# Kernel tuning notes

Hardware: AMD Instinct MI355X
Metric: run time of the kernel (lower is better)

## Reference

```python
import jax, jax.numpy as jnp
import numpy as np

HEADS = 8
BN_EPS = 1e-5

def _bn(x2d, g, b):
    # torch BatchNorm1d in training mode: biased batch stats
    mu = x2d.mean(0)
    var = x2d.var(0)
    return (x2d - mu) * jax.lax.rsqrt(var + BN_EPS) * g + b

def _window_indices(H):
    # exclusive-end box coordinates, in the exact order of the torch loop
    m = H // 2
    r0, r1, c0, c1 = [], [], [], []
    for i in range(1, m + 1):
        wins = [(m - i, m + i + 1, m - i, m + i + 1),  # full square
                (m - i, m + 1,     m - i, m + i + 1),  # top half
                (m,     m + i + 1, m - i, m + i + 1),  # bottom half
                (m - i, m + i + 1, m - i, m + 1),      # left half
                (m - i, m + i + 1, m,     m + i + 1)]  # right half
        for a, b, c, d in wins:
            r0.append(a); r1.append(b); c0.append(c); c1.append(d)
    r0 = np.array(r0); r1 = np.array(r1); c0 = np.array(c0); c1 = np.array(c1)
    counts = ((r1 - r0) * (c1 - c0)).astype(np.float32)
    return r0, r1, c0, c1, counts

def _box_sums(P, r0, r1, c0, c1):
    # P: padded 2D prefix sum [B, C, H+1, H+1]; returns [B, C, K]
    return P[:, :, r1, c1] - P[:, :, r0, c1] - P[:, :, r1, c0] + P[:, :, r0, c0]

def _integral(img):
    return jnp.pad(jnp.cumsum(jnp.cumsum(img, axis=2), axis=3), ((0, 0), (0, 0), (1, 0), (1, 0)))

def setup_inputs() -> dict:
    key = jax.random.key(0)
    ks = jax.random.split(key, 8)
    B, Cin, H = 64, 512, 31
    C = 512  # heads * base_dim
    x = jax.random.normal(ks[0], (B, Cin, H, H), dtype=jnp.float32)
    w_v = jax.random.normal(ks[1], (Cin, C), dtype=jnp.float32) * 0.02
    w_k = jax.random.normal(ks[2], (Cin, C), dtype=jnp.float32) * 0.02
    w_fc = jax.random.normal(ks[3], (Cin + C, 512), dtype=jnp.float32) * 0.02
    z = lambda n: jnp.zeros((n,), jnp.float32)
    o = lambda n: jnp.ones((n,), jnp.float32)
    return {"x": x,
            "w_v": w_v, "b_v": z(C), "g_vn": o(C), "b_vn": z(C),
            "w_k": w_k, "b_k": z(C), "g_kn": o(C), "b_kn": z(C),
            "w_fc": w_fc, "b_fc": z(512), "g_fcn": o(512), "b_fcn": z(512)}

def reference(x, w_v, b_v, g_vn, b_vn, w_k, b_k, g_kn, b_kn, w_fc, b_fc, g_fcn, b_fcn):
    B, Cin, H, W = x.shape
    N = H * W
    C = w_v.shape[1]
    d = C // HEADS
    m = H // 2
    xt = x.reshape(B, Cin, N).transpose(0, 2, 1)       # [B, N, Cin]
    x0 = xt[:, N // 2, :]                              # [B, Cin] center pixel feature
    flat = xt.reshape(B * N, Cin)
    v = jax.nn.relu(_bn(flat @ w_v + b_v, g_vn, b_vn))
    v = v.reshape(B, N, C).transpose(0, 2, 1).reshape(B, C, H, H)
    k = _bn(flat @ w_k + b_k, g_kn, b_kn).reshape(B, N, HEADS, d).transpose(0, 2, 1, 3)  # [B,h,N,d]
    q = k[:, :, N // 2, :]                             # [B, h, d]
    attn = jax.nn.softmax(jnp.einsum('bhd,bhnd->bhn', q, k) * (d ** -0.5), axis=-1)      # [B,h,N]
    attn_full = jnp.broadcast_to(attn[:, :, None, :], (B, HEADS, d, N)).reshape(B, C, H, H)
    xw = attn_full * v                                 # attn-weighted values [B,C,H,H]
    eps = 1e-16
    r0, r1, c0, c1, counts = _window_indices(H)
    Px = _integral(xw)
    Pa = _integral(attn_full)
    mx = _box_sums(Px, r0, r1, c0, c1) / counts        # window means of xw   [B,C,K]
    ma = _box_sums(Pa, r0, r1, c0, c1) / counts        # window means of attn [B,C,K]
    y_win = (mx / (ma + eps)).transpose(0, 2, 1)       # [B, K, C]
    y = jnp.concatenate([xw[:, :, m, m][:, None, :], y_win], axis=1)  # [B, n, C]
    # F.normalize(p=2, dim=2)
    y = y / jnp.maximum(jnp.linalg.norm(y, axis=2, keepdims=True), 1e-12)
    n = y.shape[1]
    yy = jnp.concatenate([jnp.broadcast_to(x0[:, None, :], (B, n, Cin)), y], axis=-1)
    out = jax.nn.relu(_bn(yy.reshape(B * n, Cin + C) @ w_fc + b_fc, g_fcn, b_fcn))
    return out.reshape(B, n, -1)
```

## Files before the change

### kernel.cpp

```cpp
#include <hip/hip_runtime.h>
#include <stdint.h>

#define DEV __device__ __forceinline__

typedef __bf16 bf16x8 __attribute__((ext_vector_type(8)));
typedef unsigned short u16x8 __attribute__((ext_vector_type(8)));
typedef float f32x4 __attribute__((ext_vector_type(4)));

DEV uint16_t f2bf(float f) {
    union { float f; uint32_t u; } v; v.f = f;
    uint32_t r = v.u + 0x7fffu + ((v.u >> 16) & 1u);
    return (uint16_t)(r >> 16);
}
DEV float bf2f(uint16_t h) {
    union { uint32_t u; float f; } v; v.u = ((uint32_t)h) << 16;
    return v.f;
}

#if __has_builtin(__builtin_amdgcn_global_load_lds)
DEV void async16(const uint16_t* g, uint16_t* l) {
    __builtin_amdgcn_global_load_lds(
        (const __attribute__((address_space(1))) uint32_t*)g,
        (__attribute__((address_space(3))) uint32_t*)l, 16, 0, 0);
}
#else
DEV void async16(const uint16_t* g, uint16_t* l) {
    *(u16x8*)l = *(const u16x8*)g;
}
#endif

__global__ void k_convert_x(const float* __restrict__ x, uint16_t* __restrict__ xbt) {
    __shared__ float tile[32][33];
    int b = blockIdx.z;
    int n0 = blockIdx.x * 32;
    int c0 = blockIdx.y * 32;
    int tx = threadIdx.x, ty = threadIdx.y;
    #pragma unroll
    for (int i = 0; i < 4; ++i) {
        int c = c0 + ty + 8 * i;
        int n = n0 + tx;
        float v = 0.f;
        if (n < 961) v = x[((size_t)b * 512 + c) * 961 + n];
        tile[ty + 8 * i][tx] = v;
    }
    __syncthreads();
    int idx = ty * 32 + tx;
    int c2 = (idx & 15) * 2;
    int nl = idx >> 4;
    #pragma unroll
    for (int i = 0; i < 2; ++i) {
        int nn = nl + 16 * i;
        int n = n0 + nn;
        if (n < 961) {
            ushort2 val;
            val.x = f2bf(tile[c2][nn]);
            val.y = f2bf(tile[c2 + 1][nn]);
            *(ushort2*)&xbt[((size_t)b * 961 + n) * 512 + c0 + c2] = val;
        }
    }
}

__global__ void k_convert_w(const float* __restrict__ wv, const float* __restrict__ wk,
                            const float* __restrict__ wfc,
                            uint16_t* __restrict__ wvkt, uint16_t* __restrict__ wfct) {
    int idx = blockIdx.x * 256 + threadIdx.x;
    if (idx < 524288) {
        int j = idx >> 9, k = idx & 511;
        float v = (j < 512) ? wv[(size_t)k * 512 + j] : wk[(size_t)k * 512 + (j - 512)];
        wvkt[idx] = f2bf(v);
    } else {
        int t = idx - 524288;
        int j = t >> 10, k = t & 1023;
        wfct[t] = f2bf(wfc[(size_t)k * 512 + j]);
    }
}

template<int K, int EPI>
__global__ __launch_bounds__(256, 4)
void k_gemm(const uint16_t* __restrict__ A, const uint16_t* __restrict__ Bt,
            int M_real,
            uint16_t* __restrict__ out_v, uint16_t* __restrict__ out_k,
            float* __restrict__ out_f,
            float* __restrict__ colsum, float* __restrict__ colsq)
{
    __shared__ __align__(16) uint16_t sbuf[16384];
    __shared__ float sStat[256];
    uint16_t* sA0 = sbuf;
    uint16_t* sA1 = sbuf + 4096;
    uint16_t* sB0 = sbuf + 8192;
    uint16_t* sB1 = sbuf + 12288;

    const int tid = threadIdx.x;
    const int wave = tid >> 6, lane = tid & 63;
    const int quad = lane >> 4, l16 = lane & 15;
    int m0, j0;
    if constexpr (EPI == 0) {
        int lin = blockIdx.x;
        int xcd = lin & 7, rest = lin >> 3;
        int jb = rest & 7, mhi = rest >> 3;
        int mb = mhi * 8 + xcd;
        if (mb >= 481) return;
        m0 = mb * 128; j0 = jb * 128;
    } else {
        m0 = blockIdx.y * 128; j0 = blockIdx.x * 128;
    }
    const int wm = wave >> 1, wj = wave & 1;

    const f32x4 fzero = {0.f, 0.f, 0.f, 0.f};
    f32x4 acc[4][4];
    #pragma unroll
    for (int i = 0; i < 4; ++i)
        #pragma unroll
        for (int j = 0; j < 4; ++j) acc[i][j] = fzero;

    const int c0 = tid;
    const int mA0 = c0 >> 2, kq0 = c0 & 3;
    const int c1 = tid + 256;
    const int mA1 = c1 >> 2, kq1 = c1 & 3;

    const int KT = K / 64;
    for (int kt = 0; kt < KT; ++kt) {
        const uint16_t* Ak = A + (size_t)m0 * K + kt * 64;
        const uint16_t* Bk = Bt + (size_t)j0 * K + kt * 64;
        async16(Ak + (size_t)mA0 * K + kq0 * 8,      &sA0[c0 * 8]);
        async16(Ak + (size_t)mA1 * K + kq1 * 8,      &sA0[c1 * 8]);
        async16(Ak + (size_t)mA0 * K + 32 + kq0 * 8, &sA1[c0 * 8]);
        async16(Ak + (size_t)mA1 * K + 32 + kq1 * 8, &sA1[c1 * 8]);
        async16(Bk + (size_t)mA0 * K + kq0 * 8,      &sB0[c0 * 8]);
        async16(Bk + (size_t)mA1 * K + kq1 * 8,      &sB0[c1 * 8]);
        async16(Bk + (size_t)mA0 * K + 32 + kq0 * 8, &sB1[c0 * 8]);
        async16(Bk + (size_t)mA1 * K + 32 + kq1 * 8, &sB1[c1 * 8]);
        __syncthreads();
        #pragma unroll
        for (int p = 0; p < 2; ++p) {
            const uint16_t* pA = p ? sA1 : sA0;
            const uint16_t* pB = p ? sB1 : sB0;
            bf16x8 af[4], bfr[4];
            #pragma unroll
            for (int i = 0; i < 4; ++i) {
                int m = wm * 64 + i * 16 + l16;
                u16x8 r = *(const u16x8*)&pA[m * 32 + quad * 8];
                af[i] = __builtin_bit_cast(bf16x8, r);
            }
            #pragma unroll
            for (int j = 0; j < 4; ++j) {
                int jj = wj * 64 + j * 16 + l16;
                u16x8 r = *(const u16x8*)&pB[jj * 32 + quad * 8];
                bfr[j] = __builtin_bit_cast(bf16x8, r);
            }
            #pragma unroll
            for (int i = 0; i < 4; ++i)
                #pragma unroll
                for (int j = 0; j < 4; ++j)
                    acc[i][j] = __builtin_amdgcn_mfma_f32_16x16x32_bf16(af[i], bfr[j], acc[i][j], 0, 0, 0);
        }
        __syncthreads();
    }

    sStat[tid] = 0.f;
    __syncthreads();

    #pragma unroll
    for (int j = 0; j < 4; ++j) {
        const int col_local = wj * 64 + j * 16 + l16;
        const int jg = j0 + col_local;
        float ls = 0.f, lq = 0.f;
        #pragma unroll
        for (int i = 0; i < 4; ++i) {
            const int rbase = m0 + wm * 64 + i * 16 + quad * 4;
            #pragma unroll
            for (int reg = 0; reg < 4; ++reg) {
                const int r = rbase + reg;
                const float val = acc[i][j][reg];
                if (r < M_real) {
                    ls += val; lq += val * val;
                    if constexpr (EPI == 1) {
                        out_f[(size_t)r * 512 + jg] = val;
                    }
                }
            }
        }
        ls += __shfl_xor(ls, 16); lq += __shfl_xor(lq, 16);
        ls += __shfl_xor(ls, 32); lq += __shfl_xor(lq, 32);
        if (quad == 0) {
            atomicAdd(&sStat[col_local], ls);
            atomicAdd(&sStat[128 + col_local], lq);
        }
    }
    __syncthreads();
    if (tid < 128) atomicAdd(&colsum[j0 + tid], sStat[tid]);
    else           atomicAdd(&colsq[j0 + (tid & 127)], sStat[tid]);

    if constexpr (EPI == 0) {
        const int rr = tid & 127;
        const int cbase = tid >> 7;
        const int r = m0 + rr;
        const bool ok = r < M_real;
        const unsigned bb_ = (unsigned)r / 961u;
        const unsigned nn = (unsigned)r - bb_ * 961u;
        #pragma unroll
        for (int ch = 0; ch < 2; ++ch) {
            if (wj == ch) {
                #pragma unroll
                for (int j = 0; j < 4; ++j) {
                    const int c = j * 16 + l16;
                    #pragma unroll
                    for (int i = 0; i < 4; ++i) {
                        const int rloc = wm * 64 + i * 16 + quad * 4;
                        union { uint16_t h[4]; uint64_t u; } p;
                        #pragma unroll
                        for (int reg = 0; reg < 4; ++reg) p.h[reg] = f2bf(acc[i][j][reg]);
                        *(uint64_t*)&sbuf[c * 136 + rloc] = p.u;
                    }
                }
            }
            __syncthreads();
            #pragma unroll
            for (int it = 0; it < 32; ++it) {
                const int c = cbase + it * 2;
                const int jg = j0 + ch * 64 + c;
                const uint16_t hv = sbuf[c * 136 + rr];
                if (ok) {
                    if (jg < 512) out_v[((size_t)bb_ * 512 + jg) * 961 + nn] = hv;
                    else          out_k[((size_t)bb_ * 512 + (jg - 512)) * 961 + nn] = hv;
                }
            }
            __syncthreads();
        }
    }
}

__global__ void k_attn(const uint16_t* __restrict__ kraw,
                       const float* __restrict__ colsum, const float* __restrict__ colsq,
                       const float* __restrict__ g_kn, const float* __restrict__ b_kn,
                       float* __restrict__ attn, float* __restrict__ maw)
{
    __shared__ float qa[64];
    __shared__ float s_qb;
    __shared__ float att[961];
    __shared__ float red[8];

    int bh = blockIdx.x;
    int b = bh >> 3, h = bh & 7;
    int tid = threadIdx.x;
    constexpr float invM = 1.f / 61504.f;

    if (tid < 64) {
        int c = h * 64 + tid;
        float mean = colsum[512 + c] * invM;
        float q_ = colsq[512 + c] * invM;
        float a = g_kn[c] * rsqrtf(q_ - mean * mean + 1e-5f);
        float bb = b_kn[c] - mean * a;
        float kr = bf2f(kraw[((size_t)b * 512 + c) * 961 + 480]);
        float qv = kr * a + bb;
        qa[tid] = qv * a;
        float qb = qv * bb;
        for (int off = 32; off; off >>= 1) qb += __shfl_down(qb, off);
        if (tid == 0) s_qb = qb;
    }
    __syncthreads();

    float lg[4];
    float lmax = -1e30f;
    #pragma unroll
    for (int it = 0; it < 4; ++it) {
        int n = tid + it * 256;
        float dot = -1e30f;
        if (n < 961) {
            const uint16_t* kp = kraw + ((size_t)b * 512 + h * 64) * 961 + n;
            float acc = 0.f;
            #pragma unroll 16
            for (int dd = 0; dd < 64; ++dd)
                acc += qa[dd] * bf2f(kp[(size_t)dd * 961]);
            dot = (acc + s_qb) * 0.125f;
        }
        lg[it] = dot;
        lmax = fmaxf(lmax, dot);
    }
    for (int off = 32; off; off >>= 1) lmax = fmaxf(lmax, __shfl_xor(lmax, off));
    if ((tid & 63) == 0) red[tid >> 6] = lmax;
    __syncthreads();
    float bmax = fmaxf(fmaxf(red[0], red[1]), fmaxf(red[2], red[3]));

    float lsum = 0.f;
    #pragma unroll
    for (int it = 0; it < 4; ++it) {
        int n = tid + it * 256;
        if (n < 961) {
            float e = __expf(lg[it] - bmax);
            lg[it] = e;
            lsum += e;
        }
    }
    for (int off = 32; off; off >>= 1) lsum += __shfl_xor(lsum, off);
    if ((tid & 63) == 0) red[4 + (tid >> 6)] = lsum;
    __syncthreads();
    float inv = 1.f / (red[4] + red[5] + red[6] + red[7]);
    #pragma unroll
    for (int it = 0; it < 4; ++it) {
        int n = tid + it * 256;
        if (n < 961) {
            float v = lg[it] * inv;
            att[n] = v;
            attn[(size_t)bh * 961 + n] = v;
        }
    }
    __syncthreads();

    if (tid < 31) { float s = 0.f; for (int cc = 0; cc < 31; ++cc) { s += att[tid * 31 + cc]; att[tid * 31 + cc] = s; } }
    __syncthreads();
    if (tid < 31) { float s = 0.f; for (int rr = 0; rr < 31; ++rr) { s += att[rr * 31 + tid]; att[rr * 31 + tid] = s; } }
    __syncthreads();

    if (tid < 75) {
        int i = tid / 5 + 1, t = tid % 5;
        const int m = 15;
        int r0, r1, cc0, cc1;
        switch (t) {
            case 0: r0 = m - i; r1 = m + i + 1; cc0 = m - i; cc1 = m + i + 1; break;
            case 1: r0 = m - i; r1 = m + 1;     cc0 = m - i; cc1 = m + i + 1; break;
            case 2: r0 = m;     r1 = m + i + 1; cc0 = m - i; cc1 = m + i + 1; break;
            case 3: r0 = m - i; r1 = m + i + 1; cc0 = m - i; cc1 = m + 1;     break;
            default:r0 = m - i; r1 = m + i + 1; cc0 = m;     cc1 = m + i + 1; break;
        }
        auto S = [&](int r, int c) -> float { return (r < 0 || c < 0) ? 0.f : att[r * 31 + c]; };
        float box = S(r1 - 1, cc1 - 1) - S(r0 - 1, cc1 - 1) - S(r1 - 1, cc0 - 1) + S(r0 - 1, cc0 - 1);
        float cnt = (float)((r1 - r0) * (cc1 - cc0));
        maw[(size_t)bh * 75 + tid] = box / cnt;
    }
}

__global__ void k_winbox(const uint16_t* __restrict__ vraw,
                         const float* __restrict__ colsum, const float* __restrict__ colsq,
                         const float* __restrict__ g_vn, const float* __restrict__ b_vn,
                         const float* __restrict__ attn, const float* __restrict__ maw,
                         float* __restrict__ y)
{
    __shared__ float xw[961];
    __shared__ float s_center;
    int bc = blockIdx.x;
    int b = bc >> 9, c = bc & 511;
    int h = c >> 6;
    int tid = threadIdx.x;
    constexpr float invM = 1.f / 61504.f;
    float mean = colsum[c] * invM;
    float q_ = colsq[c] * invM;
    float a = g_vn[c] * rsqrtf(q_ - mean * mean + 1e-5f);
    float bb = b_vn[c] - mean * a;
    const uint16_t* vp = vraw + (size_t)bc * 961;
    const float* ap = attn + (size_t)(b * 8 + h) * 961;
    for (int n = tid; n < 961; n += 128) {
        float v = fmaxf(bf2f(vp[n]) * a + bb, 0.f);
        xw[n] = v * ap[n];
    }
    __syncthreads();
    if (tid == 0) s_center = xw[480];
    __syncthreads();
    if (tid < 31) { float s = 0.f; for (int cc = 0; cc < 31; ++cc) { s += xw[tid * 31 + cc]; xw[tid * 31 + cc] = s; } }
    __syncthreads();
    if (tid < 31) { float s = 0.f; for (int rr = 0; rr < 31; ++rr) { s += xw[rr * 31 + tid]; xw[rr * 31 + tid] = s; } }
    __syncthreads();
    if (tid < 75) {
        int i = tid / 5 + 1, t = tid % 5;
        const int m = 15;
        int r0, r1, cc0, cc1;
        switch (t) {
            case 0: r0 = m - i; r1 = m + i + 1; cc0 = m - i; cc1 = m + i + 1; break;
            case 1: r0 = m - i; r1 = m + 1;     cc0 = m - i; cc1 = m + i + 1; break;
            case 2: r0 = m;     r1 = m + i + 1; cc0 = m - i; cc1 = m + i + 1; break;
            case 3: r0 = m - i; r1 = m + i + 1; cc0 = m - i; cc1 = m + 1;     break;
            default:r0 = m - i; r1 = m + i + 1; cc0 = m;     cc1 = m + i + 1; break;
        }
        auto S = [&](int r, int cc) -> float { return (r < 0 || cc < 0) ? 0.f : xw[r * 31 + cc]; };
        float box = S(r1 - 1, cc1 - 1) - S(r0 - 1, cc1 - 1) - S(r1 - 1, cc0 - 1) + S(r0 - 1, cc0 - 1);
        float cnt = (float)((r1 - r0) * (cc1 - cc0));
        float mx = box / cnt;
        float ma = maw[(size_t)(b * 8 + h) * 75 + tid];
        y[((size_t)b * 76 + 1 + tid) * 512 + c] = mx / (ma + 1e-16f);
    }
    if (tid == 96) y[((size_t)b * 76) * 512 + c] = s_center;
}

__global__ void k_build_yy(const float* __restrict__ y, const uint16_t* __restrict__ xbt,
                           uint16_t* __restrict__ yy)
{
    __shared__ float red[4];
    int row = blockIdx.x;
    int b = row / 76;
    int tid = threadIdx.x;
    const float* yp = y + (size_t)row * 512;
    float v0 = yp[tid], v1 = yp[tid + 256];
    float ss = v0 * v0 + v1 * v1;
    for (int off = 32; off; off >>= 1) ss += __shfl_xor(ss, off);
    if ((tid & 63) == 0) red[tid >> 6] = ss;
    __syncthreads();
    float tot = red[0] + red[1] + red[2] + red[3];
    float inv = 1.f / fmaxf(sqrtf(tot), 1e-12f);
    uint16_t* op = yy + (size_t)row * 1024;
    const uint16_t* x0p = xbt + ((size_t)b * 961 + 480) * 512;
    op[tid]           = x0p[tid];
    op[tid + 256]     = x0p[tid + 256];
    op[512 + tid]       = f2bf(v0 * inv);
    op[512 + tid + 256] = f2bf(v1 * inv);
}

__global__ void k_fcout(const float* __restrict__ fcraw,
                        const float* __restrict__ colsum, const float* __restrict__ colsq,
                        const float* __restrict__ g, const float* __restrict__ be,
                        float* __restrict__ out)
{
    size_t idx = (size_t)blockIdx.x * 256 + threadIdx.x;
    if (idx < (size_t)4864 * 512) {
        int j = (int)(idx & 511);
        constexpr float invM = 1.f / 4864.f;
        float mean = colsum[j] * invM;
        float q_ = colsq[j] * invM;
        float a = g[j] * rsqrtf(q_ - mean * mean + 1e-5f);
        float bb = be[j] - mean * a;
        out[idx] = fmaxf(fcraw[idx] * a + bb, 0.f);
    }
}

extern "C" void kernel_launch(void* const* d_in, const int* in_sizes, int n_in,
                              void* d_out, int out_size, void* d_ws, size_t ws_size,
                              hipStream_t stream)
{
    (void)in_sizes; (void)n_in; (void)out_size; (void)ws_size;
    const float* x    = (const float*)d_in[0];
    const float* w_v  = (const float*)d_in[1];
    const float* g_vn = (const float*)d_in[3];
    const float* b_vn = (const float*)d_in[4];
    const float* w_k  = (const float*)d_in[5];
    const float* g_kn = (const float*)d_in[7];
    const float* b_kn = (const float*)d_in[8];
    const float* w_fc = (const float*)d_in[9];
    const float* g_fcn = (const float*)d_in[11];
    const float* b_fcn = (const float*)d_in[12];
    float* out = (float*)d_out;

    char* base = (char*)d_ws;
    size_t off = 0;
    auto alloc = [&](size_t bytes) -> void* {
        void* p = base + off;
        off += (bytes + 255) & ~(size_t)255;
        return p;
    };
    uint16_t* xbt  = (uint16_t*)alloc((size_t)61568 * 512 * 2);
    uint16_t* wvkt = (uint16_t*)alloc((size_t)1024 * 512 * 2);
    uint16_t* wfct = (uint16_t*)alloc((size_t)512 * 1024 * 2);
    uint16_t* vraw = (uint16_t*)alloc((size_t)64 * 512 * 961 * 2);
    uint16_t* kraw = (uint16_t*)alloc((size_t)64 * 512 * 961 * 2);
    float* stats   = (float*)alloc(3072 * 4);
    float* attn    = (float*)alloc((size_t)64 * 8 * 961 * 4);
    float* maw     = (float*)alloc((size_t)64 * 8 * 75 * 4);
    float* y       = (float*)alloc((size_t)64 * 76 * 512 * 4);
    uint16_t* yy   = (uint16_t*)alloc((size_t)4864 * 1024 * 2);
    float* fcraw   = (float*)alloc((size_t)4864 * 512 * 4);

    hipMemsetAsync(stats, 0, 3072 * 4, stream);
    k_convert_x<<<dim3(31, 16, 64), dim3(32, 8), 0, stream>>>(x, xbt);
    k_convert_w<<<4096, 256, 0, stream>>>(w_v, w_k, w_fc, wvkt, wfct);

    k_gemm<512, 0><<<3904, 256, 0, stream>>>(xbt, wvkt, 61504, vraw, kraw, nullptr,
                                             stats, stats + 1024);

    k_attn<<<512, 256, 0, stream>>>(kraw, stats, stats + 1024, g_kn, b_kn, attn, maw);
    k_winbox<<<64 * 512, 128, 0, stream>>>(vraw, stats, stats + 1024, g_vn, b_vn, attn, maw, y);
    k_build_yy<<<4864, 256, 0, stream>>>(y, xbt, yy);

    k_gemm<1024, 1><<<dim3(4, 38), 256, 0, stream>>>(yy, wfct, 4864, nullptr, nullptr, fcraw,
                                                     stats + 2048, stats + 2560);
    k_fcout<<<9728, 256, 0, stream>>>(fcraw, stats + 2048, stats + 2560, g_fcn, b_fcn, out);
}
```

Before: 436.3 us.

## Pad spatial dimension to 968 and vectorize GEMM epilogue, attention and window loads

Pads the per-batch spatial extent from 961 to 968 in the transposed activations, the V/K buffers and the attention buffer. Every row and column count is then a multiple of 8 and the V/K GEMM has exactly 484 full tiles, so the row bounds checks go away. The V/K GEMM epilogue now writes 8-byte vectors instead of scattered 2-byte stores, and uses a packed bf16 convert. The attention and window kernels load and store four elements per thread with vector accesses, and the window kernel launches with more threads. The cost is extra padded memory and GEMM work on zero rows, which contribute nothing to the batch statistics.

After: 418.3 us. 1.04x faster.

```diff
diff --git a/kernel.cpp b/kernel.cpp
--- a/kernel.cpp
+++ b/kernel.cpp
@@ -6,6 +6,8 @@
 typedef __bf16 bf16x8 __attribute__((ext_vector_type(8)));
 typedef unsigned short u16x8 __attribute__((ext_vector_type(8)));
 typedef float f32x4 __attribute__((ext_vector_type(4)));
+
+#define NS 968
 
 DEV uint16_t f2bf(float f) {
     union { float f; uint32_t u; } v; v.f = f;
@@ -16,6 +18,20 @@
     union { uint32_t u; float f; } v; v.u = ((uint32_t)h) << 16;
     return v.f;
 }
+DEV float bflo(uint32_t w) { union { uint32_t u; float f; } v; v.u = w << 16; return v.f; }
+DEV float bfhi(uint32_t w) { union { uint32_t u; float f; } v; v.u = w & 0xffff0000u; return v.f; }
+
+#if __has_builtin(__builtin_amdgcn_cvt_pk_bf16_f32)
+typedef __bf16 bf16x2 __attribute__((ext_vector_type(2)));
+DEV uint32_t pk2bf(float lo, float hi) {
+    bf16x2 r = __builtin_amdgcn_cvt_pk_bf16_f32(lo, hi);
+    return __builtin_bit_cast(uint32_t, r);
+}
+#else
+DEV uint32_t pk2bf(float lo, float hi) {
+    return (uint32_t)f2bf(lo) | ((uint32_t)f2bf(hi) << 16);
+}
+#endif
 
 #if __has_builtin(__builtin_amdgcn_global_load_lds)
 DEV void async16(const uint16_t* g, uint16_t* l) {
@@ -45,18 +61,16 @@
     }
     __syncthreads();
     int idx = ty * 32 + tx;
-    int c2 = (idx & 15) * 2;
-    int nl = idx >> 4;
-    #pragma unroll
-    for (int i = 0; i < 2; ++i) {
-        int nn = nl + 16 * i;
-        int n = n0 + nn;
-        if (n < 961) {
-            ushort2 val;
-            val.x = f2bf(tile[c2][nn]);
-            val.y = f2bf(tile[c2 + 1][nn]);
-            *(ushort2*)&xbt[((size_t)b * 961 + n) * 512 + c0 + c2] = val;
-        }
+    int c4 = (idx & 7) * 4;
+    int nl = idx >> 3;
+    int n = n0 + nl;
+    if (n < NS) {
+        ushort4 val;
+        val.x = f2bf(tile[c4 + 0][nl]);
+        val.y = f2bf(tile[c4 + 1][nl]);
+        val.z = f2bf(tile[c4 + 2][nl]);
+        val.w = f2bf(tile[c4 + 3][nl]);
+        *(ushort4*)&xbt[((size_t)b * NS + n) * 512 + c0 + c4] = val;
     }
 }
 
@@ -78,7 +92,6 @@
 template<int K, int EPI>
 __global__ __launch_bounds__(256, 4)
 void k_gemm(const uint16_t* __restrict__ A, const uint16_t* __restrict__ Bt,
-            int M_real,
             uint16_t* __restrict__ out_v, uint16_t* __restrict__ out_k,
             float* __restrict__ out_f,
             float* __restrict__ colsum, float* __restrict__ colsq)
@@ -99,7 +112,7 @@
         int xcd = lin & 7, rest = lin >> 3;
         int jb = rest & 7, mhi = rest >> 3;
         int mb = mhi * 8 + xcd;
-        if (mb >= 481) return;
+        if (mb >= 484) return;
         m0 = mb * 128; j0 = jb * 128;
     } else {
         m0 = blockIdx.y * 128; j0 = blockIdx.x * 128;
@@ -163,20 +176,16 @@
     #pragma unroll
     for (int j = 0; j < 4; ++j) {
         const int col_local = wj * 64 + j * 16 + l16;
-        const int jg = j0 + col_local;
         float ls = 0.f, lq = 0.f;
         #pragma unroll
         for (int i = 0; i < 4; ++i) {
-            const int rbase = m0 + wm * 64 + i * 16 + quad * 4;
             #pragma unroll
             for (int reg = 0; reg < 4; ++reg) {
-                const int r = rbase + reg;
                 const float val = acc[i][j][reg];
-                if (r < M_real) {
-                    ls += val; lq += val * val;
-                    if constexpr (EPI == 1) {
-                        out_f[(size_t)r * 512 + jg] = val;
-                    }
+                ls += val; lq += val * val;
+                if constexpr (EPI == 1) {
+                    const int r = m0 + wm * 64 + i * 16 + quad * 4 + reg;
+                    out_f[(size_t)r * 512 + (j0 + col_local)] = val;
                 }
             }
         }
@@ -192,12 +201,6 @@
     else           atomicAdd(&colsq[j0 + (tid & 127)], sStat[tid]);
 
     if constexpr (EPI == 0) {
-        const int rr = tid & 127;
-        const int cbase = tid >> 7;
-        const int r = m0 + rr;
-        const bool ok = r < M_real;
-        const unsigned bb_ = (unsigned)r / 961u;
-        const unsigned nn = (unsigned)r - bb_ * 961u;
         #pragma unroll
         for (int ch = 0; ch < 2; ++ch) {
             if (wj == ch) {
@@ -207,23 +210,26 @@
                     #pragma unroll
                     for (int i = 0; i < 4; ++i) {
                         const int rloc = wm * 64 + i * 16 + quad * 4;
-                        union { uint16_t h[4]; uint64_t u; } p;
-                        #pragma unroll
-                        for (int reg = 0; reg < 4; ++reg) p.h[reg] = f2bf(acc[i][j][reg]);
-                        *(uint64_t*)&sbuf[c * 136 + rloc] = p.u;
+                        uint2 pp;
+                        pp.x = pk2bf(acc[i][j][0], acc[i][j][1]);
+                        pp.y = pk2bf(acc[i][j][2], acc[i][j][3]);
+                        *(uint2*)&sbuf[c * 136 + rloc] = pp;
                     }
                 }
             }
             __syncthreads();
+            const int jg = j0 + ch * 64;
+            uint16_t* const outp = (jg < 512) ? out_v : out_k;
+            const int jbase = (jg < 512) ? jg : jg - 512;
             #pragma unroll
-            for (int it = 0; it < 32; ++it) {
-                const int c = cbase + it * 2;
-                const int jg = j0 + ch * 64 + c;
-                const uint16_t hv = sbuf[c * 136 + rr];
-                if (ok) {
-                    if (jg < 512) out_v[((size_t)bb_ * 512 + jg) * 961 + nn] = hv;
-                    else          out_k[((size_t)bb_ * 512 + (jg - 512)) * 961 + nn] = hv;
-                }
+            for (int s = 0; s < 8; ++s) {
+                const int chunk = tid + 256 * s;
+                const int c = chunk >> 5, q = chunk & 31;
+                uint2 val = *(const uint2*)&sbuf[c * 136 + q * 4];
+                const int r = m0 + q * 4;
+                const unsigned bb_ = (unsigned)r / (unsigned)NS;
+                const unsigned nn = (unsigned)r - bb_ * (unsigned)NS;
+                *(uint2*)&outp[((size_t)bb_ * 512 + jbase + c) * NS + nn] = val;
             }
             __syncthreads();
         }
@@ -237,7 +243,7 @@
 {
     __shared__ float qa[64];
     __shared__ float s_qb;
-    __shared__ float att[961];
+    __shared__ float att[NS];
     __shared__ float red[8];
 
     int bh = blockIdx.x;
@@ -251,7 +257,7 @@
         float q_ = colsq[512 + c] * invM;
         float a = g_kn[c] * rsqrtf(q_ - mean * mean + 1e-5f);
         float bb = b_kn[c] - mean * a;
-        float kr = bf2f(kraw[((size_t)b * 512 + c) * 961 + 480]);
+        float kr = bf2f(kraw[((size_t)b * 512 + c) * NS + 480]);
         float qv = kr * a + bb;
         qa[tid] = qv * a;
         float qb = qv * bb;
@@ -260,22 +266,27 @@
     }
     __syncthreads();
 
-    float lg[4];
+    const int n4 = tid * 4;
+    const bool active = n4 < 961;
+    float a0 = 0.f, a1 = 0.f, a2 = 0.f, a3 = 0.f;
+    if (active) {
+        const uint16_t* kp = kraw + ((size_t)b * 512 + h * 64) * NS + n4;
+        #pragma unroll 16
+        for (int dd = 0; dd < 64; ++dd) {
+            uint2 kk = *(const uint2*)(kp + (size_t)dd * NS);
+            float q = qa[dd];
+            a0 += q * bflo(kk.x);
+            a1 += q * bfhi(kk.x);
+            a2 += q * bflo(kk.y);
+            a3 += q * bfhi(kk.y);
+        }
+    }
+    float lg[4] = {a0, a1, a2, a3};
     float lmax = -1e30f;
     #pragma unroll
-    for (int it = 0; it < 4; ++it) {
-        int n = tid + it * 256;
-        float dot = -1e30f;
-        if (n < 961) {
-            const uint16_t* kp = kraw + ((size_t)b * 512 + h * 64) * 961 + n;
-            float acc = 0.f;
-            #pragma unroll 16
-            for (int dd = 0; dd < 64; ++dd)
-                acc += qa[dd] * bf2f(kp[(size_t)dd * 961]);
-            dot = (acc + s_qb) * 0.125f;
-        }
-        lg[it] = dot;
-        lmax = fmaxf(lmax, dot);
+    for (int i = 0; i < 4; ++i) {
+        lg[i] = (lg[i] + s_qb) * 0.125f;
+        if (n4 + i < 961) lmax = fmaxf(lmax, lg[i]);
     }
     for (int off = 32; off; off >>= 1) lmax = fmaxf(lmax, __shfl_xor(lmax, off));
     if ((tid & 63) == 0) red[tid >> 6] = lmax;
@@ -284,26 +295,19 @@
 
     float lsum = 0.f;
     #pragma unroll
-    for (int it = 0; it < 4; ++it) {
-        int n = tid + it * 256;
-        if (n < 961) {
-            float e = __expf(lg[it] - bmax);
-            lg[it] = e;
-            lsum += e;
-        }
+    for (int i = 0; i < 4; ++i) {
+        float e = (n4 + i < 961) ? __expf(lg[i] - bmax) : 0.f;
+        lg[i] = e;
+        lsum += e;
     }
     for (int off = 32; off; off >>= 1) lsum += __shfl_xor(lsum, off);
     if ((tid & 63) == 0) red[4 + (tid >> 6)] = lsum;
     __syncthreads();
     float inv = 1.f / (red[4] + red[5] + red[6] + red[7]);
-    #pragma unroll
-    for (int it = 0; it < 4; ++it) {
-        int n = tid + it * 256;
-        if (n < 961) {
-            float v = lg[it] * inv;
-            att[n] = v;
-            attn[(size_t)bh * 961 + n] = v;
-        }
+    if (active) {
+        f32x4 v = {lg[0] * inv, lg[1] * inv, lg[2] * inv, lg[3] * inv};
+        *(f32x4*)&att[n4] = v;
+        *(f32x4*)&attn[(size_t)bh * NS + n4] = v;
     }
     __syncthreads();
 
@@ -336,7 +340,7 @@
                          const float* __restrict__ attn, const float* __restrict__ maw,
                          float* __restrict__ y)
 {
-    __shared__ float xw[961];
+    __shared__ float xw[NS];
     __shared__ float s_center;
     int bc = blockIdx.x;
     int b = bc >> 9, c = bc & 511;
@@ -347,11 +351,18 @@
     float q_ = colsq[c] * invM;
     float a = g_vn[c] * rsqrtf(q_ - mean * mean + 1e-5f);
     float bb = b_vn[c] - mean * a;
-    const uint16_t* vp = vraw + (size_t)bc * 961;
-    const float* ap = attn + (size_t)(b * 8 + h) * 961;
-    for (int n = tid; n < 961; n += 128) {
-        float v = fmaxf(bf2f(vp[n]) * a + bb, 0.f);
-        xw[n] = v * ap[n];
+    const uint16_t* vp = vraw + (size_t)bc * NS;
+    const float* ap = attn + (size_t)(b * 8 + h) * NS;
+    int n4 = tid * 4;
+    if (n4 < 961) {
+        uint2 kk = *(const uint2*)(vp + n4);
+        f32x4 at = *(const f32x4*)(ap + n4);
+        f32x4 v;
+        v[0] = fmaxf(bflo(kk.x) * a + bb, 0.f) * at[0];
+        v[1] = fmaxf(bfhi(kk.x) * a + bb, 0.f) * at[1];
+        v[2] = fmaxf(bflo(kk.y) * a + bb, 0.f) * at[2];
+        v[3] = fmaxf(bfhi(kk.y) * a + bb, 0.f) * at[3];
+        *(f32x4*)&xw[n4] = v;
     }
     __syncthreads();
     if (tid == 0) s_center = xw[480];
@@ -397,7 +408,7 @@
     float tot = red[0] + red[1] + red[2] + red[3];
     float inv = 1.f / fmaxf(sqrtf(tot), 1e-12f);
     uint16_t* op = yy + (size_t)row * 1024;
-    const uint16_t* x0p = xbt + ((size_t)b * 961 + 480) * 512;
+    const uint16_t* x0p = xbt + ((size_t)b * NS + 480) * 512;
     op[tid]           = x0p[tid];
     op[tid + 256]     = x0p[tid + 256];
     op[512 + tid]       = f2bf(v0 * inv);
@@ -445,14 +456,14 @@
         off += (bytes + 255) & ~(size_t)255;
         return p;
     };
-    uint16_t* xbt  = (uint16_t*)alloc((size_t)61568 * 512 * 2);
+    uint16_t* xbt  = (uint16_t*)alloc((size_t)64 * NS * 512 * 2);
     uint16_t* wvkt = (uint16_t*)alloc((size_t)1024 * 512 * 2);
     uint16_t* wfct = (uint16_t*)alloc((size_t)512 * 1024 * 2);
-    uint16_t* vraw = (uint16_t*)alloc((size_t)64 * 512 * 961 * 2);
-    uint16_t* kraw = (uint16_t*)alloc((size_t)64 * 512 * 961 * 2);
+    uint16_t* vraw = (uint16_t*)alloc((size_t)64 * 512 * NS * 2);
+    uint16_t* kraw = (uint16_t*)alloc((size_t)64 * 512 * NS * 2);
     float* stats   = (float*)alloc(3072 * 4);
-    float* attn    = (float*)alloc((size_t)64 * 8 * 961 * 4);
-    float* maw     = (float*)alloc((size_t)64 * 8 * 75 * 4);
+    float* attn    = (float*)alloc((size_t)512 * NS * 4);
+    float* maw     = (float*)alloc((size_t)512 * 75 * 4);
     float* y       = (float*)alloc((size_t)64 * 76 * 512 * 4);
     uint16_t* yy   = (uint16_t*)alloc((size_t)4864 * 1024 * 2);
     float* fcraw   = (float*)alloc((size_t)4864 * 512 * 4);
@@ -461,14 +472,14 @@
     k_convert_x<<<dim3(31, 16, 64), dim3(32, 8), 0, stream>>>(x, xbt);
     k_convert_w<<<4096, 256, 0, stream>>>(w_v, w_k, w_fc, wvkt, wfct);
 
-    k_gemm<512, 0><<<3904, 256, 0, stream>>>(xbt, wvkt, 61504, vraw, kraw, nullptr,
+    k_gemm<512, 0><<<3904, 256, 0, stream>>>(xbt, wvkt, vraw, kraw, nullptr,
                                              stats, stats + 1024);
 
     k_attn<<<512, 256, 0, stream>>>(kraw, stats, stats + 1024, g_kn, b_kn, attn, maw);
-    k_winbox<<<64 * 512, 128, 0, stream>>>(vraw, stats, stats + 1024, g_vn, b_vn, attn, maw, y);
+    k_winbox<<<64 * 512, 256, 0, stream>>>(vraw, stats, stats + 1024, g_vn, b_vn, attn, maw, y);
     k_build_yy<<<4864, 256, 0, stream>>>(y, xbt, yy);
 
-    k_gemm<1024, 1><<<dim3(4, 38), 256, 0, stream>>>(yy, wfct, 4864, nullptr, nullptr, fcraw,
+    k_gemm<1024, 1><<<dim3(4, 38), 256, 0, stream>>>(yy, wfct, nullptr, nullptr, fcraw,
                                                      stats + 2048, stats + 2560);
     k_fcout<<<9728, 256, 0, stream>>>(fcraw, stats + 2048, stats + 2560, g_fcn, b_fcn, out);
 }
```
